# Kernel tuning notes

Hardware: AMD Instinct MI355X
Metric: run time of the kernel (lower is better)

Reference implementation:

```python
import math
import jax, jax.numpy as jnp
import numpy as np

B, L, D, H = 8, 512, 768, 12
DK = D // H  # 64


def setup_inputs() -> dict:
    key = jax.random.key(0)
    ks = jax.random.split(key, 8)
    x = jax.random.normal(ks[0], (B, L, D), dtype=jnp.float32)
    mask = jnp.zeros((B, L), dtype=jnp.float32)            # 0 = valid, -10000 = pad (torch convention here)
    roots_label = jax.random.randint(ks[1], (B, L), 0, 2, dtype=jnp.int32)
    root_mask = jnp.ones((B, L), dtype=jnp.int32)          # only checked for not-None in the original
    W_SCALE = 0.02  # keep exp(scores) well-conditioned, as trained weights would
    Wq = jax.random.normal(ks[2], (D, D), dtype=jnp.float32) * W_SCALE
    bq = jnp.zeros((D,), dtype=jnp.float32)
    Wk = jax.random.normal(ks[3], (D, D), dtype=jnp.float32) * W_SCALE
    bk = jnp.zeros((D,), dtype=jnp.float32)
    Wr = jax.random.normal(ks[4], (D, 1), dtype=jnp.float32) * W_SCALE
    br = jnp.zeros((1,), dtype=jnp.float32)
    return {"x": x, "mask": mask, "roots_label": roots_label, "root_mask": root_mask,
            "Wq": Wq, "bq": bq, "Wk": Wk, "bk": bk, "Wr": Wr, "br": br}


def _matrix_tree_multi(scores, root):
    # scores: [B,H,L,L], root: [B,L,1]  (multi-head branch of _getMatrixTree_multi)
    A = jnp.exp(scores)                                   # [B,H,L,L]
    R = jnp.broadcast_to(jnp.exp(root)[..., 0][:, None, :], A.shape[:3])  # [B,H,L]
    col_sum = jnp.sum(A, axis=2)                          # [B,H,L]  (torch.sum(A, 2))
    eye = jnp.eye(A.shape[-1], dtype=A.dtype)
    # LL = diag(col_sum) - A + diag(R)
    LL = (col_sum + R)[..., :, None] * eye - A * (1.0 - eye) - A * eye + A * eye  # keep exact: diag(col_sum+R) - A
    LL = (col_sum + R)[..., :, None] * eye - A
    LL_inv = jnp.linalg.inv(LL)                           # [B,H,L,L]
    LL_inv_diag = jnp.diagonal(LL_inv, axis1=-2, axis2=-1)  # [B,H,L]
    d0 = R * LL_inv_diag                                  # root marginals [B,H,L]
    tmp1 = A * LL_inv_diag[..., None, :]                  # = transpose(A^T * diag[...,:,None])
    tmp2 = A * jnp.swapaxes(LL_inv, -2, -1)
    d = tmp1 - tmp2                                       # edge marginals [B,H,L,L]
    return d, d0


def reference(x, mask, roots_label, root_mask, Wq, bq, Wk, bk, Wr, br):
    key = x @ Wk + bk                                     # [B,L,D]
    query = (x @ Wq + bq) / math.sqrt(D)
    root = x @ Wr + br                                    # [B,L,1]
    q = query.reshape(B, L, H, DK).transpose(0, 2, 1, 3)  # [B,H,L,DK]
    k = key.reshape(B, L, H, DK).transpose(0, 2, 1, 3)
    scores = jnp.einsum('bhqd,bhkd->bhqk', q, k)          # [B,H,L,L]
    m = mask / -10000.0                                   # 1 at padded positions
    root = jnp.clip(root - m[:, :, None] * 50.0, -40.0, None)
    sm = jnp.broadcast_to(m[:, None, :, None], (B, H, L, L))  # scores_mask
    scores = jnp.clip(scores - sm * 50.0 - jnp.swapaxes(sm, -2, -1) * 50.0, -40.0, None)
    d, d0 = _matrix_tree_multi(scores, root)
    # root BCE loss summed over heads, masked-mean with labels
    labels = roots_label.reshape(-1).astype(jnp.float32)  # [B*L]
    p = jnp.clip(d0.astype(jnp.float32), 1e-5, 1.0 - 1e-5)
    p_h = jnp.moveaxis(p, 1, 0).reshape(H, -1)            # [H, B*L]
    bce = -(labels * jnp.log(p_h) + (1.0 - labels) * jnp.log(1.0 - p_h))
    loss_root = (bce.sum(axis=0) * labels).mean()
    attn = jnp.swapaxes(d, -2, -1)
    sm_sym = (sm + jnp.swapaxes(sm, -2, -1)).astype(bool)
    attn = jnp.where(sm_sym, 0.0, attn)
    context = jnp.einsum('bhqk,bkd->bhqd', attn, x)       # [B,H,L,D]
    return context, d, d0, loss_root
```

## Files before the change

kernel.cpp:

```cpp
#include <hip/hip_runtime.h>
#include <hip/hip_bf16.h>
#include <math.h>


#define INV_SQRT_D 0.03608439182435161f

typedef short bf16x8 __attribute__((ext_vector_type(8)));
typedef float f32x4 __attribute__((ext_vector_type(4)));
typedef unsigned int u32x4 __attribute__((ext_vector_type(4)));

__device__ __forceinline__ void mm_micro(const float* At, const float* Bt,
                                         float acc[8][8], int tx, int ty)
{
#pragma unroll
  for (int t = 0; t < 16; ++t) {
    const float4 a0 = *(const float4*)(At + t*132 + ty*8);
    const float4 a1 = *(const float4*)(At + t*132 + ty*8 + 4);
    const float4 b0 = *(const float4*)(Bt + t*132 + tx*8);
    const float4 b1 = *(const float4*)(Bt + t*132 + tx*8 + 4);
    const float a[8] = {a0.x,a0.y,a0.z,a0.w,a1.x,a1.y,a1.z,a1.w};
    const float b[8] = {b0.x,b0.y,b0.z,b0.w,b1.x,b1.y,b1.z,b1.w};
#pragma unroll
    for (int i = 0; i < 8; ++i)
#pragma unroll
      for (int j = 0; j < 8; ++j)
        acc[i][j] = fmaf(a[i], b[j], acc[i][j]);
  }
}

__global__ __launch_bounds__(256) void pack_w_kernel(
    const float* __restrict__ Wq, const float* __restrict__ Wk,
    unsigned int* __restrict__ Wqh, unsigned int* __restrict__ Wql,
    unsigned int* __restrict__ Wkh, unsigned int* __restrict__ Wkl)
{
  const int gid = blockIdx.x*256 + threadIdx.x;
  const int m = gid >= 73728;
  const int id = m ? gid - 73728 : gid;
  const int k2 = id / 192;
  const int cc = (id - k2*192) * 4;
  const float* W = m ? Wk : Wq;
  unsigned int* Oh = m ? Wkh : Wqh;
  unsigned int* Ol = m ? Wkl : Wql;
  const unsigned int* wb = (const unsigned int*)W;
  const size_t s0 = (size_t)(2*k2)*768 + cc;
  const uint4 r0 = *(const uint4*)(wb + s0);
  const uint4 r1 = *(const uint4*)(wb + s0 + 768);
  unsigned int hw[4], lw[4];
#pragma unroll
  for (int i = 0; i < 4; ++i) {
    const unsigned int u0 = ((const unsigned int*)&r0)[i];
    const unsigned int u1 = ((const unsigned int*)&r1)[i];
    const unsigned int h0 = (u0 + 0x7FFFu + ((u0 >> 16) & 1u)) >> 16;
    const unsigned int h1 = (u1 + 0x7FFFu + ((u1 >> 16) & 1u)) >> 16;
    hw[i] = h0 | (h1 << 16);
    const float rs0 = __uint_as_float(u0) - __uint_as_float(h0 << 16);
    const float rs1 = __uint_as_float(u1) - __uint_as_float(h1 << 16);
    lw[i] = __builtin_amdgcn_perm(__float_as_uint(rs1), __float_as_uint(rs0),
                                  0x07060302u);
  }
  const size_t o = (size_t)k2*768 + cc;
  *(uint4*)(Oh + o) = make_uint4(hw[0], hw[1], hw[2], hw[3]);
  *(uint4*)(Ol + o) = make_uint4(lw[0], lw[1], lw[2], lw[3]);
}

__global__ __launch_bounds__(256) void proj_mfma_kernel(
    const float* __restrict__ x,
    const unsigned int* __restrict__ Wqh, const unsigned int* __restrict__ Wql,
    const unsigned int* __restrict__ Wkh, const unsigned int* __restrict__ Wkl,
    const float* __restrict__ bq, const float* __restrict__ bk,
    float* __restrict__ Q, float* __restrict__ Kc)
{
  const unsigned int* Wh; const unsigned int* Wl;
  const float* bias; float* out; float scale;
  if (blockIdx.z == 0) { Wh = Wqh; Wl = Wql; bias = bq; out = Q;  scale = INV_SQRT_D; }
  else                 { Wh = Wkh; Wl = Wkl; bias = bk; out = Kc; scale = 1.0f; }

  const int row0 = blockIdx.y << 7;
  const int col0 = blockIdx.x << 7;

  __shared__ __align__(16) unsigned int AhL[16*132];
  __shared__ __align__(16) unsigned int AlL[16*132];
  __shared__ __align__(16) unsigned int BhL[16*132];
  __shared__ __align__(16) unsigned int BlL[16*132];

  const int tid = threadIdx.x;
  const int w = tid >> 6, l = tid & 63;
  const int wq = w >> 1, wc = w & 1;
  const int l15 = l & 15, g = l >> 4;
  const int q4 = tid & 31, pp = tid >> 5;
  const int an = tid & 127, ahh = tid >> 7;

  f32x4 acc[4][4] = {};

  for (int kk = 0; kk < 768; kk += 32) {
    __syncthreads();
#pragma unroll
    for (int s = 0; s < 2; ++s) {
      const int k2 = pp + 8*s;
      const size_t wi = (size_t)((kk >> 1) + k2)*768 + col0 + q4*4;
      *(uint4*)(BhL + k2*132 + q4*4) = *(const uint4*)(Wh + wi);
      *(uint4*)(BlL + k2*132 + q4*4) = *(const uint4*)(Wl + wi);
    }
    {
      const float* xr = x + (size_t)(row0 + an)*768 + kk + ahh*16;
      const uint4 v0 = *(const uint4*)(xr + 0);
      const uint4 v1 = *(const uint4*)(xr + 4);
      const uint4 v2 = *(const uint4*)(xr + 8);
      const uint4 v3 = *(const uint4*)(xr + 12);
      const unsigned int uu[16] = {v0.x,v0.y,v0.z,v0.w, v1.x,v1.y,v1.z,v1.w,
                                   v2.x,v2.y,v2.z,v2.w, v3.x,v3.y,v3.z,v3.w};
#pragma unroll
      for (int pr = 0; pr < 8; ++pr) {
        const unsigned int a0 = uu[2*pr], a1 = uu[2*pr+1];
        const unsigned int hw = __builtin_amdgcn_perm(a1, a0, 0x07060302u);
        const float f0 = __uint_as_float(a0) - __uint_as_float(a0 & 0xffff0000u);
        const float f1 = __uint_as_float(a1) - __uint_as_float(a1 & 0xffff0000u);
        const unsigned int lw = __builtin_amdgcn_perm(__float_as_uint(f1),
                                                      __float_as_uint(f0),
                                                      0x07060302u);
        const int k2 = ahh*8 + pr;
        AhL[k2*132 + an] = hw;
        AlL[k2*132 + an] = lw;
      }
    }
    __syncthreads();

    u32x4 ah[4], al[4], bhv[4], blv[4];
#pragma unroll
    for (int mi = 0; mi < 4; ++mi) {
      const int col = wq*64 + mi*16 + l15;
#pragma unroll
      for (int d2 = 0; d2 < 4; ++d2) {
        ah[mi][d2] = AhL[(4*g + d2)*132 + col];
        al[mi][d2] = AlL[(4*g + d2)*132 + col];
      }
    }
#pragma unroll
    for (int ni = 0; ni < 4; ++ni) {
      const int col = wc*64 + ni*16 + l15;
#pragma unroll
      for (int d2 = 0; d2 < 4; ++d2) {
        bhv[ni][d2] = BhL[(4*g + d2)*132 + col];
        blv[ni][d2] = BlL[(4*g + d2)*132 + col];
      }
    }

#pragma unroll
    for (int mi = 0; mi < 4; ++mi) {
      const bf16x8 Ah = __builtin_bit_cast(bf16x8, ah[mi]);
      const bf16x8 Al = __builtin_bit_cast(bf16x8, al[mi]);
#pragma unroll
      for (int ni = 0; ni < 4; ++ni) {
        const bf16x8 Bh = __builtin_bit_cast(bf16x8, bhv[ni]);
        const bf16x8 Bl = __builtin_bit_cast(bf16x8, blv[ni]);
        acc[mi][ni] = __builtin_amdgcn_mfma_f32_16x16x32_bf16(Ah, Bh, acc[mi][ni], 0, 0, 0);
        acc[mi][ni] = __builtin_amdgcn_mfma_f32_16x16x32_bf16(Ah, Bl, acc[mi][ni], 0, 0, 0);
        acc[mi][ni] = __builtin_amdgcn_mfma_f32_16x16x32_bf16(Al, Bh, acc[mi][ni], 0, 0, 0);
      }
    }
  }

#pragma unroll
  for (int mi = 0; mi < 4; ++mi) {
    const int row = row0 + wq*64 + mi*16 + g*4;
#pragma unroll
    for (int ni = 0; ni < 4; ++ni) {
      const int col = col0 + wc*64 + ni*16 + l15;
      const float bs = bias[col];
#pragma unroll
      for (int r = 0; r < 4; ++r)
        out[(size_t)(row + r)*768 + col] = (acc[mi][ni][r] + bs) * scale;
    }
  }
}

__global__ __launch_bounds__(256) void root_kernel(
    const float* __restrict__ x, const float* __restrict__ Wr,
    const float* __restrict__ br, const float* __restrict__ mask,
    float* __restrict__ Rv, float* __restrict__ mv)
{
  const int n = blockIdx.x*4 + (threadIdx.x >> 6);
  const int lane = threadIdx.x & 63;
  float s = 0.0f;
  for (int c = lane; c < 768; c += 64) s += x[(size_t)n*768 + c] * Wr[c];
#pragma unroll
  for (int off = 32; off > 0; off >>= 1) s += __shfl_down(s, off, 64);
  if (lane == 0) {
    const float root = s + br[0];
    const float m = mask[n] * (-1e-4f);
    Rv[n] = expf(fmaxf(root - m*50.0f, -40.0f));
    mv[n] = m;
  }
}

__global__ __launch_bounds__(256) void scores_kernel(
    const float* __restrict__ Qs, const float* __restrict__ Ks,
    const float* __restrict__ mv, float* __restrict__ A)
{
  const int bh = blockIdx.z, b = bh / 12, h = bh % 12;
  const int i0 = blockIdx.y * 128, j0 = blockIdx.x * 128;
  __shared__ __align__(16) float At[16*132];
  __shared__ __align__(16) float Bt[16*132];
  const int tx = threadIdx.x, ty = threadIdx.y;
  const int tid = ty*16 + tx;
  const int lt = tid & 15, lr = tid >> 4;
  const size_t qbase = (size_t)(b*512 + i0)*768 + h*64;
  const size_t kbase = (size_t)(b*512 + j0)*768 + h*64;

  float acc[8][8] = {};

  for (int kk = 0; kk < 64; kk += 16) {
#pragma unroll
    for (int u = 0; u < 8; ++u) {
      const int r = lr + 16*u;
      At[lt*132 + r] = Qs[qbase + (size_t)r*768 + kk + lt];
      Bt[lt*132 + r] = Ks[kbase + (size_t)r*768 + kk + lt];
    }
    __syncthreads();
    mm_micro(At, Bt, acc, tx, ty);
    __syncthreads();
  }

  float mi[8], mj[8];
#pragma unroll
  for (int i = 0; i < 8; ++i) mi[i] = mv[b*512 + i0 + ty*8 + i];
#pragma unroll
  for (int j = 0; j < 8; ++j) mj[j] = mv[b*512 + j0 + tx*8 + j];

#pragma unroll
  for (int i = 0; i < 8; ++i) {
    const size_t rowb = (size_t)(bh*512 + i0 + ty*8 + i)*512;
#pragma unroll
    for (int j = 0; j < 8; j += 4) {
      float4 v;
      v.x = expf(fmaxf(acc[i][j+0] - (mi[i]+mj[j+0])*50.0f, -40.0f));
      v.y = expf(fmaxf(acc[i][j+1] - (mi[i]+mj[j+1])*50.0f, -40.0f));
      v.z = expf(fmaxf(acc[i][j+2] - (mi[i]+mj[j+2])*50.0f, -40.0f));
      v.w = expf(fmaxf(acc[i][j+3] - (mi[i]+mj[j+3])*50.0f, -40.0f));
      *(float4*)(A + rowb + j0 + tx*8 + j) = v;
    }
  }
}

__global__ __launch_bounds__(256) void pack_x_kernel(
    const float* __restrict__ x, unsigned int* __restrict__ xh,
    unsigned int* __restrict__ xl)
{
  const int gid = blockIdx.x*256 + threadIdx.x;
  const int k2g = gid / 192;
  const int cc  = (gid - k2g*192) * 4;
  const unsigned int* xb = (const unsigned int*)x;
  const size_t s0 = (size_t)(2*k2g)*768 + cc;
  const uint4 r0 = *(const uint4*)(xb + s0);
  const uint4 r1 = *(const uint4*)(xb + s0 + 768);
  unsigned int hw[4], lw[4];
#pragma unroll
  for (int i = 0; i < 4; ++i) {
    const unsigned int u0 = ((const unsigned int*)&r0)[i];
    const unsigned int u1 = ((const unsigned int*)&r1)[i];
    const unsigned int h0 = (u0 + 0x7FFFu + ((u0 >> 16) & 1u)) >> 16;
    const unsigned int h1 = (u1 + 0x7FFFu + ((u1 >> 16) & 1u)) >> 16;
    hw[i] = h0 | (h1 << 16);
    const float rs0 = __uint_as_float(u0) - __uint_as_float(h0 << 16);
    const float rs1 = __uint_as_float(u1) - __uint_as_float(h1 << 16);
    lw[i] = __builtin_amdgcn_perm(__float_as_uint(rs1), __float_as_uint(rs0),
                                  0x07060302u);
  }
  const size_t o = (size_t)k2g*768 + cc;
  *(uint4*)(xh + o) = make_uint4(hw[0], hw[1], hw[2], hw[3]);
  *(uint4*)(xl + o) = make_uint4(lw[0], lw[1], lw[2], lw[3]);
}

__global__ void colsum_kernel(const float* __restrict__ A, float* __restrict__ colsum)
{
  const int bh = blockIdx.y;
  const int j = blockIdx.x*256 + threadIdx.x;
  const float* Ab = A + (size_t)bh*262144;
  float s = 0.0f;
  for (int i = 0; i < 512; ++i) s += Ab[(size_t)i*512 + j];
  colsum[bh*512 + j] = s;
}

__global__ void buildM_kernel(const float* __restrict__ A, const float* __restrict__ colsum,
                              const float* __restrict__ Rv, float* __restrict__ M)
{
  const size_t g = ((size_t)blockIdx.x*256 + threadIdx.x)*4;
  const int bh = (int)(g >> 18);
  const int i = (int)((g >> 9) & 511);
  const int j = (int)(g & 511);
  const float4 a = *(const float4*)(A + g);
  float4 v; v.x = -a.x; v.y = -a.y; v.z = -a.z; v.w = -a.w;
  if (i >= j && i < j+4) {
    const float dadd = colsum[bh*512 + i] + Rv[(bh/12)*512 + i];
    ((float*)&v)[i - j] += dadd;
  }
  *(float4*)(M + g) = v;
}

__global__ __launch_bounds__(64) void gj_inv_kernel(
    const float* __restrict__ M, float* __restrict__ Inv, int k0)
{
  const float* const Mg = M + (size_t)blockIdx.x * 262144;
  float* const Ig = Inv + (size_t)blockIdx.x * 4096;
  const int lane = threadIdx.x;

  float w[64];
  {
    const float* src = Mg + (size_t)(k0 + lane)*512 + k0;
#pragma unroll
    for (int q = 0; q < 16; ++q) {
      const float4 t4 = *(const float4*)(src + q*4);
      w[q*4+0]=t4.x; w[q*4+1]=t4.y; w[q*4+2]=t4.z; w[q*4+3]=t4.w;
    }
  }

  float fcur = w[0];
#pragma unroll 1
  for (int kk = 0; kk < 64; ++kk) {
    float rj[64];
#pragma unroll
    for (int j = 0; j < 64; ++j) rj[j] = __shfl(w[j], kk);
    const float pv = __shfl(fcur, kk);
    const float p  = 1.0f / pv;
    const bool isp = (lane == kk);
    const float alpha = isp ? p : -fcur * p;
    float fnext = fcur;
#pragma unroll
    for (int j = 0; j < 64; ++j) {
      const float base = isp ? 0.0f : w[j];
      float val = fmaf(alpha, rj[j], base);
      if (j == kk) val = alpha;
      w[j] = val;
      if (j == kk + 1) fnext = val;
    }
    fcur = fnext;
  }

  {
    float* dst = Ig + lane*64;
#pragma unroll
    for (int q = 0; q < 16; ++q)
      *(float4*)(dst + q*4) = make_float4(w[q*4+0], w[q*4+1], w[q*4+2], w[q*4+3]);
  }
}

__global__ __launch_bounds__(256) void gj_w_kernel(
    float* __restrict__ M, float* __restrict__ Mp,
    const float* __restrict__ Inv, int k0)
{
  const int bh = blockIdx.y;
  const int row0 = blockIdx.x * 128;
  float* const Mg = M + (size_t)bh*262144;
  float* const Mpg = Mp + (size_t)bh*32768;
  const float* const Ig = Inv + (size_t)bh*4096;

  __shared__ __align__(16) float Ct[16*132];
  __shared__ __align__(16) float It[16*68];

  const int tx = threadIdx.x, ty = threadIdx.y;
  const int tid = ty*16 + tx;
  const int lt = tid & 15, lr = tid >> 4;

  {
    const int rq = blockIdx.x;
    const int c4 = (tid & 127) * 4;
    const int rr = tid >> 7;
#pragma unroll
    for (int u = 0; u < 8; ++u) {
      const int r = rq*16 + u*2 + rr;
      *(float4*)(Mpg + (size_t)r*512 + c4) =
          *(const float4*)(Mg + (size_t)(k0 + r)*512 + c4);
    }
  }

  float acc[8][4] = {};

  for (int kc = 0; kc < 64; kc += 16) {
#pragma unroll
    for (int u = 0; u < 8; ++u) {
      const int r = lr + 16*u;
      Ct[lt*132 + r] = Mg[(size_t)(row0 + r)*512 + k0 + kc + lt];
    }
    {
      const int j = tid & 63, t0 = tid >> 6;
#pragma unroll
      for (int u = 0; u < 4; ++u) {
        const int t = t0*4 + u;
        It[t*68 + j] = Ig[(kc + t)*64 + j];
      }
    }
    __syncthreads();
#pragma unroll
    for (int t = 0; t < 16; ++t) {
      const float4 a0 = *(const float4*)(Ct + t*132 + ty*8);
      const float4 a1 = *(const float4*)(Ct + t*132 + ty*8 + 4);
      const float4 b  = *(const float4*)(It + t*68 + tx*4);
      const float a[8] = {a0.x,a0.y,a0.z,a0.w,a1.x,a1.y,a1.z,a1.w};
      const float bb[4] = {b.x,b.y,b.z,b.w};
#pragma unroll
      for (int i = 0; i < 8; ++i)
#pragma unroll
        for (int j = 0; j < 4; ++j)
          acc[i][j] = fmaf(a[i], bb[j], acc[i][j]);
    }
    __syncthreads();
  }

#pragma unroll
  for (int i = 0; i < 8; ++i) {
    const int irow = row0 + ty*8 + i;
    float4 v;
    if (irow >= k0 && irow < k0 + 64) {
      v = *(const float4*)(Ig + (irow - k0)*64 + tx*4);
    } else {
      v = make_float4(-acc[i][0], -acc[i][1], -acc[i][2], -acc[i][3]);
    }
    *(float4*)(Mg + (size_t)irow*512 + k0 + tx*4) = v;
  }
}

__global__ __launch_bounds__(256) void gj_update_kernel(
    float* __restrict__ M, const float* __restrict__ Mp, int k0)
{
  const int bh = blockIdx.z;
  const int row0 = blockIdx.y * 128, col0 = blockIdx.x * 128;
  float* const Mg = M + (size_t)bh*262144;
  const float* const Mpg = Mp + (size_t)bh*32768;

  __shared__ __align__(16) float At[16*132];
  __shared__ __align__(16) float Bt[16*132];
  const int tx = threadIdx.x, ty = threadIdx.y;
  const int tid = ty*16 + tx;
  const int lt = tid & 15, lr = tid >> 4;
  const int bc = tid & 127, btr = tid >> 7;

  float acc[8][8] = {};

  for (int kc = 0; kc < 64; kc += 16) {
#pragma unroll
    for (int u = 0; u < 8; ++u) {
      const int r = lr + 16*u;
      At[lt*132 + r] = Mg[(size_t)(row0 + r)*512 + k0 + kc + lt];
    }
#pragma unroll
    for (int u = 0; u < 8; ++u) {
      const int t = btr + 2*u;
      Bt[t*132 + bc] = Mpg[(size_t)(kc + t)*512 + col0 + bc];
    }
    __syncthreads();
    mm_micro(At, Bt, acc, tx, ty);
    __syncthreads();
  }

#pragma unroll
  for (int ii = 0; ii < 8; ++ii) {
    const int irow = row0 + ty*8 + ii;
    const bool inP = (irow >= k0) && (irow < k0 + 64);
#pragma unroll
    for (int jj = 0; jj < 8; jj += 4) {
      const int jcol = col0 + tx*8 + jj;
      if (jcol >= k0 && jcol < k0 + 64) continue;
      float* cell = Mg + (size_t)irow*512 + jcol;
      float4 v = make_float4(acc[ii][jj+0], acc[ii][jj+1], acc[ii][jj+2], acc[ii][jj+3]);
      if (!inP) {
        const float4 o = *(const float4*)cell;
        v.x += o.x; v.y += o.y; v.z += o.z; v.w += o.w;
      }
      *(float4*)cell = v;
    }
  }
}

__global__ void diag_d0_kernel(const float* __restrict__ Minv, const float* __restrict__ Rv,
                               float* __restrict__ diagv, float* __restrict__ d0)
{
  const int bh = blockIdx.x, l = threadIdx.x;
  const float dg = Minv[(size_t)bh*262144 + (size_t)l*513];
  diagv[bh*512 + l] = dg;
  d0[bh*512 + l] = Rv[(bh/12)*512 + l] * dg;
}

__global__ __launch_bounds__(1024) void loss_kernel(const float* __restrict__ d0,
                                                    const int* __restrict__ labels,
                                                    float* __restrict__ loss)
{
  float acc = 0.0f;
  for (int n = threadIdx.x; n < 4096; n += 1024) {
    if (labels[n] != 0) {
      const int b = n >> 9, l = n & 511;
      float s = 0.0f;
#pragma unroll
      for (int h = 0; h < 12; ++h) {
        float p = d0[(size_t)(b*12 + h)*512 + l];
        p = fminf(fmaxf(p, 1e-5f), 1.0f - 1e-5f);
        s -= logf(p);
      }
      acc += s;
    }
  }
  __shared__ float red[16];
#pragma unroll
  for (int off = 32; off > 0; off >>= 1) acc += __shfl_down(acc, off, 64);
  const int wv = threadIdx.x >> 6, ln = threadIdx.x & 63;
  if (ln == 0) red[wv] = acc;
  __syncthreads();
  if (threadIdx.x == 0) {
    float t = 0.0f;
    for (int w2 = 0; w2 < 16; ++w2) t += red[w2];
    loss[0] = t * (1.0f/4096.0f);
  }
}

__global__ __launch_bounds__(256) void finalize_d_kernel(
    float* __restrict__ dmat, const float* __restrict__ Minv, const float* __restrict__ diagv)
{
  const int bh = blockIdx.z;
  const int i0 = blockIdx.y*64, j0 = blockIdx.x*64;
  __shared__ float t[64][65];
  const int tx = threadIdx.x, ty = threadIdx.y;
  const size_t mbase = (size_t)bh*262144;
  for (int jj = ty; jj < 64; jj += 4)
    t[jj][tx] = Minv[mbase + (size_t)(j0+jj)*512 + i0 + tx];
  __syncthreads();
  const float dg_j = diagv[bh*512 + j0 + tx];
  for (int ii = ty; ii < 64; ii += 4) {
    const size_t idx = mbase + (size_t)(i0+ii)*512 + j0 + tx;
    dmat[idx] = dmat[idx] * (dg_j - t[tx][ii]);
  }
}

__global__ __launch_bounds__(256) void context_packed_kernel(
    const float* __restrict__ dmat, const unsigned int* __restrict__ xh,
    const unsigned int* __restrict__ xl, const float* __restrict__ mv,
    float* __restrict__ ctx)
{
  const int bh = blockIdx.z + 8, b = bh / 12;
  const int q0 = blockIdx.y << 7;
  const int c0 = blockIdx.x << 7;

  __shared__ __align__(16) unsigned int AhL[16*132];
  __shared__ __align__(16) unsigned int AlL[16*132];
  __shared__ __align__(16) unsigned int BhL[16*132];
  __shared__ __align__(16) unsigned int BlL[16*132];

  const int tid = threadIdx.x;
  const int w = tid >> 6, l = tid & 63;
  const int wq = w >> 1, wc = w & 1;
  const int l15 = l & 15, g = l >> 4;
  const int q4 = tid & 31, pp = tid >> 5;

  const size_t dbase = (size_t)bh*262144;
  const int xrow0 = b*256;

  float mq[4];
  {
    const float4 t4 = *(const float4*)(mv + b*512 + q0 + q4*4);
    mq[0]=t4.x; mq[1]=t4.y; mq[2]=t4.z; mq[3]=t4.w;
  }

  f32x4 acc[4][4] = {};

  for (int kk = 0; kk < 512; kk += 32) {
    __syncthreads();
#pragma unroll
    for (int s = 0; s < 2; ++s) {
      const int k2 = pp + 8*s;
      const int krow = kk + 2*k2;
      const float mk0 = mv[b*512 + krow];
      const float mk1 = mv[b*512 + krow + 1];
      const uint4 r0 = *(const uint4*)(dmat + dbase + (size_t)krow*512 + q0 + q4*4);
      const uint4 r1 = *(const uint4*)(dmat + dbase + (size_t)(krow+1)*512 + q0 + q4*4);
      unsigned int hw[4], lw[4];
#pragma unroll
      for (int i = 0; i < 4; ++i) {
        unsigned int v0 = ((const unsigned int*)&r0)[i];
        unsigned int v1 = ((const unsigned int*)&r1)[i];
        v0 = ((mk0 + mq[i]) != 0.0f) ? 0u : v0;
        v1 = ((mk1 + mq[i]) != 0.0f) ? 0u : v1;
        hw[i] = __builtin_amdgcn_perm(v1, v0, 0x07060302u);
        const float f0 = __uint_as_float(v0) - __uint_as_float(v0 & 0xffff0000u);
        const float f1 = __uint_as_float(v1) - __uint_as_float(v1 & 0xffff0000u);
        lw[i] = __builtin_amdgcn_perm(__float_as_uint(f1), __float_as_uint(f0),
                                      0x07060302u);
      }
      *(uint4*)(AhL + k2*132 + q4*4) = make_uint4(hw[0], hw[1], hw[2], hw[3]);
      *(uint4*)(AlL + k2*132 + q4*4) = make_uint4(lw[0], lw[1], lw[2], lw[3]);
      const size_t xi = (size_t)(xrow0 + (kk >> 1) + k2)*768 + c0 + q4*4;
      *(uint4*)(BhL + k2*132 + q4*4) = *(const uint4*)(xh + xi);
      *(uint4*)(BlL + k2*132 + q4*4) = *(const uint4*)(xl + xi);
    }
    __syncthreads();

    u32x4 ah[4], al[4], bhv[4], blv[4];
#pragma unroll
    for (int mi = 0; mi < 4; ++mi) {
      const int col = wq*64 + mi*16 + l15;
#pragma unroll
      for (int d2 = 0; d2 < 4; ++d2) {
        ah[mi][d2] = AhL[(4*g + d2)*132 + col];
        al[mi][d2] = AlL[(4*g + d2)*132 + col];
      }
    }
#pragma unroll
    for (int ni = 0; ni < 4; ++ni) {
      const int col = wc*64 + ni*16 + l15;
#pragma unroll
      for (int d2 = 0; d2 < 4; ++d2) {
        bhv[ni][d2] = BhL[(4*g + d2)*132 + col];
        blv[ni][d2] = BlL[(4*g + d2)*132 + col];
      }
    }

#pragma unroll
    for (int mi = 0; mi < 4; ++mi) {
      const bf16x8 Ah = __builtin_bit_cast(bf16x8, ah[mi]);
      const bf16x8 Al = __builtin_bit_cast(bf16x8, al[mi]);
#pragma unroll
      for (int ni = 0; ni < 4; ++ni) {
        const bf16x8 Bh = __builtin_bit_cast(bf16x8, bhv[ni]);
        const bf16x8 Bl = __builtin_bit_cast(bf16x8, blv[ni]);
        acc[mi][ni] = __builtin_amdgcn_mfma_f32_16x16x32_bf16(Ah, Bh, acc[mi][ni], 0, 0, 0);
        acc[mi][ni] = __builtin_amdgcn_mfma_f32_16x16x32_bf16(Ah, Bl, acc[mi][ni], 0, 0, 0);
        acc[mi][ni] = __builtin_amdgcn_mfma_f32_16x16x32_bf16(Al, Bh, acc[mi][ni], 0, 0, 0);
      }
    }
  }

#pragma unroll
  for (int mi = 0; mi < 4; ++mi) {
    const int row = q0 + wq*64 + mi*16 + g*4;
#pragma unroll
    for (int ni = 0; ni < 4; ++ni) {
      const int col = c0 + wc*64 + ni*16 + l15;
#pragma unroll
      for (int r = 0; r < 4; ++r)
        ctx[((size_t)bh*512 + row + r)*768 + col] = acc[mi][ni][r];
    }
  }
}

__device__ __forceinline__ unsigned int pack_bf16x2(float v)
{
  const unsigned int u = __float_as_uint(v);
  const unsigned int hi = (u + 0x7FFFu + ((u >> 16) & 1u)) >> 16;
  const float hf = __uint_as_float(hi << 16);
  const unsigned int lo = __float_as_uint(v - hf) >> 16;
  return hi | (lo << 16);
}

__global__ __launch_bounds__(256) void context_mfma_kernel(
    const float* __restrict__ dmat, const float* __restrict__ x,
    const float* __restrict__ mv, float* __restrict__ ctx)
{
  const int bh = blockIdx.z, b = bh / 12;
  const int q0 = blockIdx.y << 7;
  const int c0 = blockIdx.x << 7;

  __shared__ unsigned int As[32*133];
  __shared__ unsigned int Bs[32*133];

  const int tid = threadIdx.x;
  const int w = tid >> 6, l = tid & 63;
  const int wq = w >> 1, wc = w & 1;
  const int l15 = l & 15, g = l >> 4;
  const int q4 = tid & 31, kr0 = tid >> 5;

  const size_t dbase = (size_t)bh*262144;
  const size_t xbase = (size_t)b*393216;

  float mq[4];
  {
    const float4 t4 = *(const float4*)(mv + b*512 + q0 + q4*4);
    mq[0]=t4.x; mq[1]=t4.y; mq[2]=t4.z; mq[3]=t4.w;
  }

  f32x4 acc[4][4] = {};

  for (int kk = 0; kk < 512; kk += 32) {
    __syncthreads();
#pragma unroll
    for (int p = 0; p < 4; ++p) {
      const int kr = kr0 + 8*p;
      const int krow = kk + kr;
      const float mk = mv[b*512 + krow];
      const float4 av = *(const float4*)(dmat + dbase + (size_t)krow*512 + q0 + q4*4);
      const float4 bv = *(const float4*)(x + xbase + (size_t)krow*768 + c0 + q4*4);
      unsigned int* aw = As + kr*133 + q4*4;
      unsigned int* bw = Bs + kr*133 + q4*4;
      aw[0] = pack_bf16x2(((mk + mq[0]) != 0.0f) ? 0.0f : av.x);
      aw[1] = pack_bf16x2(((mk + mq[1]) != 0.0f) ? 0.0f : av.y);
      aw[2] = pack_bf16x2(((mk + mq[2]) != 0.0f) ? 0.0f : av.z);
      aw[3] = pack_bf16x2(((mk + mq[3]) != 0.0f) ? 0.0f : av.w);
      bw[0] = pack_bf16x2(bv.x);
      bw[1] = pack_bf16x2(bv.y);
      bw[2] = pack_bf16x2(bv.z);
      bw[3] = pack_bf16x2(bv.w);
    }
    __syncthreads();

    u32x4 ah[4], al[4], bhv[4], blv[4];
#pragma unroll
    for (int mi = 0; mi < 4; ++mi) {
      const unsigned int* base = As + g*8*133 + (wq*64 + mi*16 + l15);
      unsigned int u[8];
#pragma unroll
      for (int e = 0; e < 8; ++e) u[e] = base[e*133];
#pragma unroll
      for (int d2 = 0; d2 < 4; ++d2) {
        ah[mi][d2] = __builtin_amdgcn_perm(u[2*d2+1], u[2*d2], 0x05040100u);
        al[mi][d2] = __builtin_amdgcn_perm(u[2*d2+1], u[2*d2], 0x07060302u);
      }
    }
#pragma unroll
    for (int ni = 0; ni < 4; ++ni) {
      const unsigned int* base = Bs + g*8*133 + (wc*64 + ni*16 + l15);
      unsigned int u[8];
#pragma unroll
      for (int e = 0; e < 8; ++e) u[e] = base[e*133];
#pragma unroll
      for (int d2 = 0; d2 < 4; ++d2) {
        bhv[ni][d2] = __builtin_amdgcn_perm(u[2*d2+1], u[2*d2], 0x05040100u);
        blv[ni][d2] = __builtin_amdgcn_perm(u[2*d2+1], u[2*d2], 0x07060302u);
      }
    }

#pragma unroll
    for (int mi = 0; mi < 4; ++mi) {
      const bf16x8 Ah = __builtin_bit_cast(bf16x8, ah[mi]);
      const bf16x8 Al = __builtin_bit_cast(bf16x8, al[mi]);
#pragma unroll
      for (int ni = 0; ni < 4; ++ni) {
        const bf16x8 Bh = __builtin_bit_cast(bf16x8, bhv[ni]);
        const bf16x8 Bl = __builtin_bit_cast(bf16x8, blv[ni]);
        acc[mi][ni] = __builtin_amdgcn_mfma_f32_16x16x32_bf16(Ah, Bh, acc[mi][ni], 0, 0, 0);
        acc[mi][ni] = __builtin_amdgcn_mfma_f32_16x16x32_bf16(Ah, Bl, acc[mi][ni], 0, 0, 0);
        acc[mi][ni] = __builtin_amdgcn_mfma_f32_16x16x32_bf16(Al, Bh, acc[mi][ni], 0, 0, 0);
      }
    }
  }

#pragma unroll
  for (int mi = 0; mi < 4; ++mi) {
    const int row = q0 + wq*64 + mi*16 + g*4;
#pragma unroll
    for (int ni = 0; ni < 4; ++ni) {
      const int col = c0 + wc*64 + ni*16 + l15;
#pragma unroll
      for (int r = 0; r < 4; ++r)
        ctx[((size_t)bh*512 + row + r)*768 + col] = acc[mi][ni][r];
    }
  }
}

extern "C" void kernel_launch(void* const* d_in, const int* in_sizes, int n_in,
                              void* d_out, int out_size, void* d_ws, size_t ws_size,
                              hipStream_t stream)
{
  (void)in_sizes; (void)n_in; (void)out_size; (void)ws_size;

  const float* x    = (const float*)d_in[0];
  const float* mask = (const float*)d_in[1];
  const int*   roots= (const int*)d_in[2];
  const float* Wq   = (const float*)d_in[4];
  const float* bq   = (const float*)d_in[5];
  const float* Wk   = (const float*)d_in[6];
  const float* bk   = (const float*)d_in[7];
  const float* Wr   = (const float*)d_in[8];
  const float* br   = (const float*)d_in[9];

  float* out        = (float*)d_out;
  float* ctx_region = out;
  float* d_region   = out + 37748736;
  float* d0_region  = out + 62914560;
  float* loss_ptr   = out + 62963712;

  float* Qs = ctx_region;
  float* Ks = ctx_region + 3145728;
  float* Mv = ctx_region + 6291456;
  float* Mp = ctx_region + 31457280;
  float* Invs = ctx_region + 34603008;

  unsigned int* xh = (unsigned int*)ctx_region;
  unsigned int* xl = (unsigned int*)ctx_region + 1572864;

  unsigned int* Wqh = (unsigned int*)ctx_region + 34996224;
  unsigned int* Wql = Wqh + 294912;
  unsigned int* Wkh = Wql + 294912;
  unsigned int* Wkl = Wkh + 294912;

  float* ws     = (float*)d_ws;
  float* Rv     = ws;
  float* mv     = ws + 4096;
  float* colsum = ws + 8192;
  float* diagv  = ws + 57344;

  pack_w_kernel <<<dim3(576),     dim3(256),   0, stream>>>(Wq, Wk, Wqh, Wql, Wkh, Wkl);
  proj_mfma_kernel<<<dim3(6,32,2), dim3(256),  0, stream>>>(x, Wqh, Wql, Wkh, Wkl, bq, bk, Qs, Ks);
  root_kernel   <<<dim3(1024),    dim3(256),   0, stream>>>(x, Wr, br, mask, Rv, mv);
  scores_kernel <<<dim3(4,4,96),  dim3(16,16), 0, stream>>>(Qs, Ks, mv, d_region);
  pack_x_kernel <<<dim3(1536),    dim3(256),   0, stream>>>(x, xh, xl);
  colsum_kernel <<<dim3(2,96),    dim3(256),   0, stream>>>(d_region, colsum);
  buildM_kernel <<<dim3(24576),   dim3(256),   0, stream>>>(d_region, colsum, Rv, Mv);

  for (int step = 0; step < 8; ++step) {
    const int k0 = step * 64;
    gj_inv_kernel   <<<dim3(96),     dim3(64),    0, stream>>>(Mv, Invs, k0);
    gj_w_kernel     <<<dim3(4,96),   dim3(16,16), 0, stream>>>(Mv, Mp, Invs, k0);
    gj_update_kernel<<<dim3(4,4,96), dim3(16,16), 0, stream>>>(Mv, Mp, k0);
  }

  diag_d0_kernel<<<dim3(96),      dim3(512),   0, stream>>>(Mv, Rv, diagv, d0_region);
  loss_kernel   <<<dim3(1),       dim3(1024),  0, stream>>>(d0_region, roots, loss_ptr);
  finalize_d_kernel<<<dim3(8,8,96), dim3(64,4), 0, stream>>>(d_region, Mv, diagv);
  context_packed_kernel<<<dim3(6,4,88), dim3(256), 0, stream>>>(d_region, xh, xl, mv, ctx_region);
  context_mfma_kernel  <<<dim3(6,4,8),  dim3(256), 0, stream>>>(d_region, x, mv, ctx_region);
}
```

Before: 1.863 ms.

## Move Gauss-Jordan trailing update to split-bf16 MFMA and stream pivot-row shuffles

Replaces the FP32 FMA tiled rank-64 update in the blocked Gauss-Jordan inversion with an MFMA kernel. Each FP32 operand is split into high and low bf16 parts, and three bf16 MFMAs per tile emulate near-FP32 precision. The pivot-inverse kernel also stops buffering the 64-entry shuffled pivot row in registers and shuffles per element, which lowers register pressure. The split-bf16 trick drops the low*low term, so the inversion may accumulate more rounding error across the 8 blocked steps.

```diff
diff --git a/kernel.cpp b/kernel.cpp
--- a/kernel.cpp
+++ b/kernel.cpp
@@ -8,6 +8,15 @@
 typedef short bf16x8 __attribute__((ext_vector_type(8)));
 typedef float f32x4 __attribute__((ext_vector_type(4)));
 typedef unsigned int u32x4 __attribute__((ext_vector_type(4)));
+
+__device__ __forceinline__ void packpair(unsigned int v0, unsigned int v1,
+                                         unsigned int& hw, unsigned int& lw)
+{
+  hw = __builtin_amdgcn_perm(v1, v0, 0x07060302u);
+  const float f0 = __uint_as_float(v0) - __uint_as_float(v0 & 0xffff0000u);
+  const float f1 = __uint_as_float(v1) - __uint_as_float(v1 & 0xffff0000u);
+  lw = __builtin_amdgcn_perm(__float_as_uint(f1), __float_as_uint(f0), 0x07060302u);
+}
 
 __device__ __forceinline__ void mm_micro(const float* At, const float* Bt,
                                          float acc[8][8], int tx, int ty)
@@ -111,13 +120,8 @@
                                    v2.x,v2.y,v2.z,v2.w, v3.x,v3.y,v3.z,v3.w};
 #pragma unroll
       for (int pr = 0; pr < 8; ++pr) {
-        const unsigned int a0 = uu[2*pr], a1 = uu[2*pr+1];
-        const unsigned int hw = __builtin_amdgcn_perm(a1, a0, 0x07060302u);
-        const float f0 = __uint_as_float(a0) - __uint_as_float(a0 & 0xffff0000u);
-        const float f1 = __uint_as_float(a1) - __uint_as_float(a1 & 0xffff0000u);
-        const unsigned int lw = __builtin_amdgcn_perm(__float_as_uint(f1),
-                                                      __float_as_uint(f0),
-                                                      0x07060302u);
+        unsigned int hw, lw;
+        packpair(uu[2*pr], uu[2*pr+1], hw, lw);
         const int k2 = ahh*8 + pr;
         AhL[k2*132 + an] = hw;
         AlL[k2*132 + an] = lw;
@@ -317,21 +321,19 @@
   float fcur = w[0];
 #pragma unroll 1
   for (int kk = 0; kk < 64; ++kk) {
-    float rj[64];
-#pragma unroll
-    for (int j = 0; j < 64; ++j) rj[j] = __shfl(w[j], kk);
     const float pv = __shfl(fcur, kk);
     const float p  = 1.0f / pv;
     const bool isp = (lane == kk);
-    const float alpha = isp ? p : -fcur * p;
+    const float fp = (isp ? (pv - 1.0f) : fcur) * p;
+    const float pivfix = isp ? p : -fp;
     float fnext = fcur;
 #pragma unroll
     for (int j = 0; j < 64; ++j) {
-      const float base = isp ? 0.0f : w[j];
-      float val = fmaf(alpha, rj[j], base);
-      if (j == kk) val = alpha;
+      const float rj = __shfl(w[j], kk);
+      float val = fmaf(-fp, rj, w[j]);
+      if (j == kk) val = pivfix;
+      if (j == kk + 1) fnext = val;
       w[j] = val;
-      if (j == kk + 1) fnext = val;
     }
     fcur = fnext;
   }
@@ -419,54 +421,113 @@
   }
 }
 
-__global__ __launch_bounds__(256) void gj_update_kernel(
+__global__ __launch_bounds__(256) void gj_update_mfma_kernel(
     float* __restrict__ M, const float* __restrict__ Mp, int k0)
 {
   const int bh = blockIdx.z;
-  const int row0 = blockIdx.y * 128, col0 = blockIdx.x * 128;
+  const int row0 = blockIdx.y << 7, col0 = blockIdx.x << 7;
   float* const Mg = M + (size_t)bh*262144;
   const float* const Mpg = Mp + (size_t)bh*32768;
 
-  __shared__ __align__(16) float At[16*132];
-  __shared__ __align__(16) float Bt[16*132];
-  const int tx = threadIdx.x, ty = threadIdx.y;
-  const int tid = ty*16 + tx;
-  const int lt = tid & 15, lr = tid >> 4;
-  const int bc = tid & 127, btr = tid >> 7;
-
-  float acc[8][8] = {};
-
-  for (int kc = 0; kc < 64; kc += 16) {
-#pragma unroll
-    for (int u = 0; u < 8; ++u) {
-      const int r = lr + 16*u;
-      At[lt*132 + r] = Mg[(size_t)(row0 + r)*512 + k0 + kc + lt];
-    }
-#pragma unroll
-    for (int u = 0; u < 8; ++u) {
-      const int t = btr + 2*u;
-      Bt[t*132 + bc] = Mpg[(size_t)(kc + t)*512 + col0 + bc];
-    }
-    __syncthreads();
-    mm_micro(At, Bt, acc, tx, ty);
-    __syncthreads();
-  }
-
-#pragma unroll
-  for (int ii = 0; ii < 8; ++ii) {
-    const int irow = row0 + ty*8 + ii;
-    const bool inP = (irow >= k0) && (irow < k0 + 64);
-#pragma unroll
-    for (int jj = 0; jj < 8; jj += 4) {
-      const int jcol = col0 + tx*8 + jj;
-      if (jcol >= k0 && jcol < k0 + 64) continue;
-      float* cell = Mg + (size_t)irow*512 + jcol;
-      float4 v = make_float4(acc[ii][jj+0], acc[ii][jj+1], acc[ii][jj+2], acc[ii][jj+3]);
-      if (!inP) {
-        const float4 o = *(const float4*)cell;
-        v.x += o.x; v.y += o.y; v.z += o.z; v.w += o.w;
-      }
-      *(float4*)cell = v;
+  __shared__ __align__(16) unsigned int AhL[16*132];
+  __shared__ __align__(16) unsigned int AlL[16*132];
+  __shared__ __align__(16) unsigned int BhL[16*132];
+  __shared__ __align__(16) unsigned int BlL[16*132];
+
+  const int tid = threadIdx.x;
+  const int w = tid >> 6, l = tid & 63;
+  const int wq = w >> 1, wc = w & 1;
+  const int l15 = l & 15, g = l >> 4;
+  const int q4 = tid & 31, pp = tid >> 5;
+  const int an = tid & 127, ahh = tid >> 7;
+
+  f32x4 acc[4][4] = {};
+
+  for (int kc = 0; kc < 64; kc += 32) {
+    __syncthreads();
+#pragma unroll
+    for (int s = 0; s < 2; ++s) {
+      const int k2 = pp + 8*s;
+      const int krow = kc + 2*k2;
+      const uint4 r0 = *(const uint4*)((const unsigned int*)Mpg + (size_t)krow*512 + col0 + q4*4);
+      const uint4 r1 = *(const uint4*)((const unsigned int*)Mpg + (size_t)(krow+1)*512 + col0 + q4*4);
+      unsigned int hw[4], lw[4];
+#pragma unroll
+      for (int i = 0; i < 4; ++i)
+        packpair(((const unsigned int*)&r0)[i], ((const unsigned int*)&r1)[i], hw[i], lw[i]);
+      *(uint4*)(BhL + k2*132 + q4*4) = make_uint4(hw[0], hw[1], hw[2], hw[3]);
+      *(uint4*)(BlL + k2*132 + q4*4) = make_uint4(lw[0], lw[1], lw[2], lw[3]);
+    }
+    {
+      const float* ar = Mg + (size_t)(row0 + an)*512 + k0 + kc + ahh*16;
+      const uint4 v0 = *(const uint4*)(ar + 0);
+      const uint4 v1 = *(const uint4*)(ar + 4);
+      const uint4 v2 = *(const uint4*)(ar + 8);
+      const uint4 v3 = *(const uint4*)(ar + 12);
+      const unsigned int uu[16] = {v0.x,v0.y,v0.z,v0.w, v1.x,v1.y,v1.z,v1.w,
+                                   v2.x,v2.y,v2.z,v2.w, v3.x,v3.y,v3.z,v3.w};
+#pragma unroll
+      for (int pr = 0; pr < 8; ++pr) {
+        unsigned int hw, lw;
+        packpair(uu[2*pr], uu[2*pr+1], hw, lw);
+        const int k2 = ahh*8 + pr;
+        AhL[k2*132 + an] = hw;
+        AlL[k2*132 + an] = lw;
+      }
+    }
+    __syncthreads();
+
+    u32x4 ah[4], al[4], bhv[4], blv[4];
+#pragma unroll
+    for (int mi = 0; mi < 4; ++mi) {
+      const int col = wq*64 + mi*16 + l15;
+#pragma unroll
+      for (int d2 = 0; d2 < 4; ++d2) {
+        ah[mi][d2] = AhL[(4*g + d2)*132 + col];
+        al[mi][d2] = AlL[(4*g + d2)*132 + col];
+      }
+    }
+#pragma unroll
+    for (int ni = 0; ni < 4; ++ni) {
+      const int col = wc*64 + ni*16 + l15;
+#pragma unroll
+      for (int d2 = 0; d2 < 4; ++d2) {
+        bhv[ni][d2] = BhL[(4*g + d2)*132 + col];
+        blv[ni][d2] = BlL[(4*g + d2)*132 + col];
+      }
+    }
+
+#pragma unroll
+    for (int mi = 0; mi < 4; ++mi) {
+      const bf16x8 Ah = __builtin_bit_cast(bf16x8, ah[mi]);
+      const bf16x8 Al = __builtin_bit_cast(bf16x8, al[mi]);
+#pragma unroll
+      for (int ni = 0; ni < 4; ++ni) {
+        const bf16x8 Bh = __builtin_bit_cast(bf16x8, bhv[ni]);
+        const bf16x8 Bl = __builtin_bit_cast(bf16x8, blv[ni]);
+        acc[mi][ni] = __builtin_amdgcn_mfma_f32_16x16x32_bf16(Ah, Bh, acc[mi][ni], 0, 0, 0);
+        acc[mi][ni] = __builtin_amdgcn_mfma_f32_16x16x32_bf16(Ah, Bl, acc[mi][ni], 0, 0, 0);
+        acc[mi][ni] = __builtin_amdgcn_mfma_f32_16x16x32_bf16(Al, Bh, acc[mi][ni], 0, 0, 0);
+      }
+    }
+  }
+
+  const int col_base = col0 + wc*64;
+  if (col_base == k0) return;
+  const int row_base = row0 + wq*64;
+  const bool inP = (row_base == k0);
+#pragma unroll
+  for (int mi = 0; mi < 4; ++mi) {
+#pragma unroll
+    for (int ni = 0; ni < 4; ++ni) {
+      const int col = col_base + ni*16 + l15;
+#pragma unroll
+      for (int r = 0; r < 4; ++r) {
+        float* cell = Mg + (size_t)(row_base + mi*16 + g*4 + r)*512 + col;
+        float v = acc[mi][ni][r];
+        if (!inP) v += *cell;
+        *cell = v;
+      }
     }
   }
 }
@@ -577,11 +638,7 @@
         unsigned int v1 = ((const unsigned int*)&r1)[i];
         v0 = ((mk0 + mq[i]) != 0.0f) ? 0u : v0;
         v1 = ((mk1 + mq[i]) != 0.0f) ? 0u : v1;
-        hw[i] = __builtin_amdgcn_perm(v1, v0, 0x07060302u);
-        const float f0 = __uint_as_float(v0) - __uint_as_float(v0 & 0xffff0000u);
-        const float f1 = __uint_as_float(v1) - __uint_as_float(v1 & 0xffff0000u);
-        lw[i] = __builtin_amdgcn_perm(__float_as_uint(f1), __float_as_uint(f0),
-                                      0x07060302u);
+        packpair(v0, v1, hw[i], lw[i]);
       }
       *(uint4*)(AhL + k2*132 + q4*4) = make_uint4(hw[0], hw[1], hw[2], hw[3]);
       *(uint4*)(AlL + k2*132 + q4*4) = make_uint4(lw[0], lw[1], lw[2], lw[3]);
@@ -804,9 +861,9 @@
 
   for (int step = 0; step < 8; ++step) {
     const int k0 = step * 64;
-    gj_inv_kernel   <<<dim3(96),     dim3(64),    0, stream>>>(Mv, Invs, k0);
-    gj_w_kernel     <<<dim3(4,96),   dim3(16,16), 0, stream>>>(Mv, Mp, Invs, k0);
-    gj_update_kernel<<<dim3(4,4,96), dim3(16,16), 0, stream>>>(Mv, Mp, k0);
+    gj_inv_kernel        <<<dim3(96),     dim3(64),    0, stream>>>(Mv, Invs, k0);
+    gj_w_kernel          <<<dim3(4,96),   dim3(16,16), 0, stream>>>(Mv, Mp, Invs, k0);
+    gj_update_mfma_kernel<<<dim3(4,4,96), dim3(256),   0, stream>>>(Mv, Mp, k0);
   }
 
   diag_d0_kernel<<<dim3(96),      dim3(512),   0, stream>>>(Mv, Rv, diagv, d0_region);
```

After: 1.926 ms. 1.03x slower.
